# Performance work log

Hardware: AMD Instinct MI355X
Metric: run time of the kernel (lower is better)

## Reference

```python
import jax, jax.numpy as jnp
import numpy as np

B = 128
K = 16
# (in_ch, featdim, dim) per stage, matching conv1..conv11
DIMS = [(3, 8, 2048), (8, 32, 1024), (32, 64, 512), (64, 64, 256), (64, 64, 128),
        (64, 128, 64), (128, 256, 32), (256, 512, 16), (512, 512, 8), (512, 512, 4),
        (512, 1024, 2)]


def setup_inputs() -> dict:
    key = jax.random.key(0)
    ks = jax.random.split(key, 64)
    inp = {"x": jax.random.normal(ks[0], (B, 3, 2048), dtype=jnp.float32)}
    i = 1
    for li, (cin, cf, d) in enumerate(DIMS, start=1):
        inp[f"W{li}"] = jax.random.normal(ks[i], (3 * cf, cin), dtype=jnp.float32) / np.sqrt(cin).astype(np.float32); i += 1
        inp[f"b{li}"] = jax.random.normal(ks[i], (3 * cf,), dtype=jnp.float32) * 0.01; i += 1
        inp[f"sel{li}"] = jax.random.randint(ks[i], (d,), 0, 3); i += 1
    inp["fcW"] = jax.random.normal(ks[i], (K, 1024), dtype=jnp.float32) / np.sqrt(1024).astype(np.float32); i += 1
    inp["fcb"] = jax.random.normal(ks[i], (K,), dtype=jnp.float32) * 0.01
    return inp


def kdconv(x, W, b, sel, featdim, dim):
    # 1x1 conv == per-position matmul: x [B, Cin, dim] -> y [B, 3*featdim, dim]
    y = jax.nn.relu(jnp.einsum('oi,bin->bon', W, x) + b[None, :, None])
    y = y.reshape(-1, featdim, 3, dim)
    # kd split-dim gather: pick one of the 3 feature groups per position
    y = jnp.take_along_axis(y, sel[None, None, None, :], axis=2)[:, :, 0, :]  # [B, featdim, dim]
    # pairwise max-pool of sibling leaves
    return y.reshape(-1, featdim, dim // 2, 2).max(axis=-1)  # [B, featdim, dim//2]


def reference(x, sel1, sel2, sel3, sel4, sel5, sel6, sel7, sel8, sel9, sel10, sel11,
              W1, b1, W2, b2, W3, b3, W4, b4, W5, b5, W6, b6, W7, b7, W8, b8,
              W9, b9, W10, b10, W11, b11, fcW, fcb):
    Ws = [W1, W2, W3, W4, W5, W6, W7, W8, W9, W10, W11]
    bs = [b1, b2, b3, b4, b5, b6, b7, b8, b9, b10, b11]
    sels = [sel1, sel2, sel3, sel4, sel5, sel6, sel7, sel8, sel9, sel10, sel11]
    h = x
    for (cin, cf, d), W, b, s in zip(DIMS, Ws, bs, sels):
        h = kdconv(h, W, b, s, cf, d)
    h = h.reshape(-1, 1024)  # [B, 1024]
    return jax.nn.log_softmax(h @ fcW.T + fcb, axis=-1)
```

## Files before the change

kernel.cpp:

```cpp
#include <hip/hip_runtime.h>
#include <math.h>

typedef __attribute__((ext_vector_type(8))) short bf16x8;
typedef __attribute__((ext_vector_type(4))) float f32x4;

__device__ __forceinline__ unsigned short f2bf(float f) {
    unsigned u = __builtin_bit_cast(unsigned, f);
    u += 0x7FFF + ((u >> 16) & 1);
    return (unsigned short)(u >> 16);
}
__device__ __forceinline__ float bf2f(unsigned short h) {
    unsigned u = ((unsigned)h) << 16;
    return __builtin_bit_cast(float, u);
}

struct K1Params {
    const float* x;
    const float* W1; const float* B1; const int* S1;
    const float* W2; const float* B2; const int* S2;
    const float* Wsrc[9];
    unsigned short* Wb;
    unsigned short* X3;
};

__global__ __launch_bounds__(256) void k1_kernel(K1Params P)
{
    const int tid = threadIdx.x;

    if (blockIdx.x >= 128) {
        int gt = (blockIdx.x - 128) * 256 + tid;
        const int we[9] = {6144, 12288, 12288, 24576, 98304, 393216, 786432, 786432, 1572864};
        int off = 0;
#pragma unroll
        for (int li = 0; li < 9; ++li) {
            const float4* src = (const float4*)P.Wsrc[li];
            ushort4* dst = (ushort4*)(P.Wb + off);
            int n4 = we[li] >> 2;
            for (int i = gt; i < n4; i += 32768) {
                float4 w = src[i];
                dst[i] = make_ushort4(f2bf(w.x), f2bf(w.y), f2bf(w.z), f2bf(w.w));
            }
            off += we[li];
        }
        return;
    }

    __shared__ float wl1[72], bl1[24], wl2[768], bl2[96];
    __shared__ unsigned short bufL1[16 * 64 * 8];

    if (tid < 72) wl1[tid] = P.W1[tid];
    if (tid >= 128 && tid < 152) bl1[tid - 128] = P.B1[tid - 128];
    for (int i = tid; i < 768; i += 256) wl2[i] = P.W2[i];
    if (tid < 96) bl2[tid] = P.B2[tid];
    __syncthreads();

    const int npT = blockIdx.x >> 1;
    const int b0  = (blockIdx.x & 1) * 64;

    for (int i = tid; i < 1024; i += 256) {
        int pos_l = i >> 6, bl = i & 63;
        int np1 = npT * 16 + pos_l;
        int b = b0 + bl;
        int s0 = P.S1[2 * np1], s1 = P.S1[2 * np1 + 1];
        const float* xb = P.x + (size_t)b * 6144 + 2 * np1;
        float2 c0 = *(const float2*)(xb);
        float2 c1 = *(const float2*)(xb + 2048);
        float2 c2 = *(const float2*)(xb + 4096);
        unsigned short o[8];
#pragma unroll
        for (int f = 0; f < 8; ++f) {
            int r0 = f * 3 + s0, r1 = f * 3 + s1;
            float z0 = fmaf(wl1[r0*3+2], c2.x, fmaf(wl1[r0*3+1], c1.x, fmaf(wl1[r0*3+0], c0.x, bl1[r0])));
            float z1 = fmaf(wl1[r1*3+2], c2.y, fmaf(wl1[r1*3+1], c1.y, fmaf(wl1[r1*3+0], c0.y, bl1[r1])));
            o[f] = f2bf(fmaxf(fmaxf(z0, z1), 0.f));
        }
        unsigned short* dst = &bufL1[((size_t)pos_l * 64 + bl) * 8];
        *(ushort4*)dst       = make_ushort4(o[0], o[1], o[2], o[3]);
        *(ushort4*)(dst + 4) = make_ushort4(o[4], o[5], o[6], o[7]);
    }
    __syncthreads();

    for (int i = tid; i < 512; i += 256) {
        int np_l = i >> 6, bl = i & 63;
        int np2 = npT * 8 + np_l;
        int s0 = P.S2[2 * np2], s1 = P.S2[2 * np2 + 1];
        const unsigned short* r0 = &bufL1[((size_t)(2 * np_l) * 64 + bl) * 8];
        const unsigned short* r1 = &bufL1[((size_t)(2 * np_l + 1) * 64 + bl) * 8];
        float xa[8], xb[8];
        {
            ushort4 u0 = *(const ushort4*)r0, u1 = *(const ushort4*)(r0 + 4);
            ushort4 v0 = *(const ushort4*)r1, v1 = *(const ushort4*)(r1 + 4);
            xa[0]=bf2f(u0.x); xa[1]=bf2f(u0.y); xa[2]=bf2f(u0.z); xa[3]=bf2f(u0.w);
            xa[4]=bf2f(u1.x); xa[5]=bf2f(u1.y); xa[6]=bf2f(u1.z); xa[7]=bf2f(u1.w);
            xb[0]=bf2f(v0.x); xb[1]=bf2f(v0.y); xb[2]=bf2f(v0.z); xb[3]=bf2f(v0.w);
            xb[4]=bf2f(v1.x); xb[5]=bf2f(v1.y); xb[6]=bf2f(v1.z); xb[7]=bf2f(v1.w);
        }
        unsigned short o[32];
#pragma unroll
        for (int f = 0; f < 32; ++f) {
            const float* w0 = &wl2[(f * 3 + s0) * 8];
            const float* w1 = &wl2[(f * 3 + s1) * 8];
            float z0 = bl2[f * 3 + s0], z1 = bl2[f * 3 + s1];
#pragma unroll
            for (int k = 0; k < 8; ++k) {
                z0 = fmaf(w0[k], xa[k], z0);
                z1 = fmaf(w1[k], xb[k], z1);
            }
            o[f] = f2bf(fmaxf(fmaxf(z0, z1), 0.f));
        }
        unsigned short* dst = P.X3 + ((size_t)np2 * 128 + b0 + bl) * 32;
#pragma unroll
        for (int i2 = 0; i2 < 8; ++i2)
            *(ushort4*)(dst + 4 * i2) = make_ushort4(o[4*i2], o[4*i2+1], o[4*i2+2], o[4*i2+3]);
    }
}

template<int CIN>
__device__ __forceinline__ void mfma_tile(
    const unsigned short* a0, const unsigned short* a1,
    const unsigned short* b0p, const unsigned short* b1p,
    f32x4& acc0, f32x4& acc1)
{
#pragma unroll
    for (int k = 0; k < CIN; k += 32) {
        bf16x8 A0 = __builtin_bit_cast(bf16x8, *(const float4*)(const void*)(a0 + k));
        bf16x8 A1 = __builtin_bit_cast(bf16x8, *(const float4*)(const void*)(a1 + k));
        bf16x8 B0 = __builtin_bit_cast(bf16x8, *(const float4*)(const void*)(b0p + k));
        bf16x8 B1 = __builtin_bit_cast(bf16x8, *(const float4*)(const void*)(b1p + k));
        acc0 = __builtin_amdgcn_mfma_f32_16x16x32_bf16(A0, B0, acc0, 0, 0, 0);
        acc1 = __builtin_amdgcn_mfma_f32_16x16x32_bf16(A1, B1, acc1, 0, 0, 0);
    }
}

template<int CIN, int RPE>
__device__ __forceinline__ void mfma_tile_lds(
    const unsigned short* a0, const unsigned short* a1,
    const unsigned short* b0p, const unsigned short* b1p,
    f32x4& acc0, f32x4& acc1)
{
#pragma unroll
    for (int k = 0; k < CIN; k += 32) {
        bf16x8 A0 = __builtin_bit_cast(bf16x8, *(const float4*)(const void*)(a0 + k));
        bf16x8 A1 = __builtin_bit_cast(bf16x8, *(const float4*)(const void*)(a1 + k));
        bf16x8 B0 = __builtin_bit_cast(bf16x8, *(const float4*)(const void*)(b0p + k));
        bf16x8 B1 = __builtin_bit_cast(bf16x8, *(const float4*)(const void*)(b1p + k));
        acc0 = __builtin_amdgcn_mfma_f32_16x16x32_bf16(A0, B0, acc0, 0, 0, 0);
        acc1 = __builtin_amdgcn_mfma_f32_16x16x32_bf16(A1, B1, acc1, 0, 0, 0);
    }
}

__device__ __forceinline__ void epilogue_store(
    unsigned short* dst, const f32x4& acc0, const f32x4& acc1,
    const float* bias, int fbase, int s0, int s1)
{
    unsigned short o[4];
#pragma unroll
    for (int r = 0; r < 4; ++r) {
        float v = fmaxf(fmaxf(acc0[r] + bias[(fbase + r) * 3 + s0],
                              acc1[r] + bias[(fbase + r) * 3 + s1]), 0.f);
        o[r] = f2bf(v);
    }
    *(ushort4*)dst = make_ushort4(o[0], o[1], o[2], o[3]);
}

__global__ __launch_bounds__(256) void stage2_kernel(
    const unsigned short* __restrict__ X3,
    const unsigned short* __restrict__ Wb,
    const float* __restrict__ B3, const int* __restrict__ S3,
    const float* __restrict__ B4, const int* __restrict__ S4,
    const float* __restrict__ B5, const int* __restrict__ S5,
    unsigned short* __restrict__ X6)
{
    constexpr int RPE = 72;
    __shared__ unsigned short L3o[4 * 32 * RPE];
    __shared__ unsigned short L4o[2 * 32 * RPE];

    const int tid  = threadIdx.x;
    const int lane = tid & 63;
    const int wv   = tid >> 6;
    const int c = lane & 15, q = lane >> 4;
    const int n5 = blockIdx.x >> 2;
    const int b0 = (blockIdx.x & 3) * 32;

    const unsigned short* W3b = Wb;
    const unsigned short* W4b = Wb + 6144;
    const unsigned short* W5b = Wb + 18432;

    for (int t = wv; t < 32; t += 4) {
        int bt = t & 1, ft = (t >> 1) & 3, j = t >> 3;
        int np = 4 * n5 + j;
        int s0 = __builtin_amdgcn_readfirstlane(S3[2 * np]);
        int s1 = __builtin_amdgcn_readfirstlane(S3[2 * np + 1]);
        int f0 = ft * 16, bl = bt * 16;
        const unsigned short* a0 = W3b + (size_t)((f0 + c) * 3 + s0) * 32 + q * 8;
        const unsigned short* a1 = W3b + (size_t)((f0 + c) * 3 + s1) * 32 + q * 8;
        const unsigned short* bp0 = X3 + ((size_t)(8 * n5 + 2 * j) * 128 + b0 + bl + c) * 32 + q * 8;
        const unsigned short* bp1 = X3 + ((size_t)(8 * n5 + 2 * j + 1) * 128 + b0 + bl + c) * 32 + q * 8;
        f32x4 acc0 = {0.f,0.f,0.f,0.f}, acc1 = {0.f,0.f,0.f,0.f};
        mfma_tile<32>(a0, a1, bp0, bp1, acc0, acc1);
        epilogue_store(&L3o[((size_t)j * 32 + bl + c) * RPE + f0 + q * 4],
                       acc0, acc1, B3, f0 + q * 4, s0, s1);
    }
    __syncthreads();

    for (int t = wv; t < 16; t += 4) {
        int bt = t & 1, ft = (t >> 1) & 3, j = t >> 3;
        int np = 2 * n5 + j;
        int s0 = __builtin_amdgcn_readfirstlane(S4[2 * np]);
        int s1 = __builtin_amdgcn_readfirstlane(S4[2 * np + 1]);
        int f0 = ft * 16, bl = bt * 16;
        const unsigned short* a0 = W4b + (size_t)((f0 + c) * 3 + s0) * 64 + q * 8;
        const unsigned short* a1 = W4b + (size_t)((f0 + c) * 3 + s1) * 64 + q * 8;
        const unsigned short* bp0 = &L3o[((size_t)(2 * j) * 32 + bl + c) * RPE + q * 8];
        const unsigned short* bp1 = &L3o[((size_t)(2 * j + 1) * 32 + bl + c) * RPE + q * 8];
        f32x4 acc0 = {0.f,0.f,0.f,0.f}, acc1 = {0.f,0.f,0.f,0.f};
        mfma_tile_lds<64, RPE>(a0, a1, bp0, bp1, acc0, acc1);
        epilogue_store(&L4o[((size_t)j * 32 + bl + c) * RPE + f0 + q * 4],
                       acc0, acc1, B4, f0 + q * 4, s0, s1);
    }
    __syncthreads();

    for (int t = wv; t < 8; t += 4) {
        int bt = t & 1, ft = t >> 1;
        int s0 = __builtin_amdgcn_readfirstlane(S5[2 * n5]);
        int s1 = __builtin_amdgcn_readfirstlane(S5[2 * n5 + 1]);
        int f0 = ft * 16, bl = bt * 16;
        const unsigned short* a0 = W5b + (size_t)((f0 + c) * 3 + s0) * 64 + q * 8;
        const unsigned short* a1 = W5b + (size_t)((f0 + c) * 3 + s1) * 64 + q * 8;
        const unsigned short* bp0 = &L4o[((size_t)(0) * 32 + bl + c) * RPE + q * 8];
        const unsigned short* bp1 = &L4o[((size_t)(1) * 32 + bl + c) * RPE + q * 8];
        f32x4 acc0 = {0.f,0.f,0.f,0.f}, acc1 = {0.f,0.f,0.f,0.f};
        mfma_tile_lds<64, RPE>(a0, a1, bp0, bp1, acc0, acc1);
        epilogue_store(X6 + ((size_t)n5 * 128 + b0 + bl + c) * 64 + f0 + q * 4,
                       acc0, acc1, B5, f0 + q * 4, s0, s1);
    }
}

template<int CIN, int CF, int NP, int MW, int NW>
__global__ __launch_bounds__(256) void mfma_kernel(
    const unsigned short* __restrict__ Xin,
    const unsigned short* __restrict__ Wb,
    const float* __restrict__ bias,
    const int*   __restrict__ sel,
    unsigned short* __restrict__ Xout)
{
    constexpr int FT = CF / (16 * MW);
    constexpr int BT = 128 / (16 * NW);

    const int wid  = threadIdx.x >> 6;
    const int lane = threadIdx.x & 63;
    const int task = blockIdx.x * 4 + wid;
    const int bi = task % BT;
    const int fi = (task / BT) % FT;
    const int n  = task / (BT * FT);

    const int c = lane & 15;
    const int q = lane >> 4;
    const int s0 = __builtin_amdgcn_readfirstlane(sel[2 * n]);
    const int s1 = __builtin_amdgcn_readfirstlane(sel[2 * n + 1]);

    const int f0 = fi * 16 * MW;
    const int b0 = bi * 16 * NW;

    const unsigned short* ap[2][MW];
    const unsigned short* bp[2][NW];
#pragma unroll
    for (int p = 0; p < 2; ++p) {
        int s = p ? s1 : s0;
#pragma unroll
        for (int mi = 0; mi < MW; ++mi)
            ap[p][mi] = Wb + (size_t)((f0 + mi * 16 + c) * 3 + s) * CIN + q * 8;
#pragma unroll
        for (int ni = 0; ni < NW; ++ni)
            bp[p][ni] = Xin + ((size_t)(2 * n + p) * 128 + b0 + ni * 16 + c) * CIN + q * 8;
    }

    f32x4 acc[2][MW][NW];
#pragma unroll
    for (int p = 0; p < 2; ++p)
#pragma unroll
        for (int mi = 0; mi < MW; ++mi)
#pragma unroll
            for (int ni = 0; ni < NW; ++ni)
                acc[p][mi][ni] = (f32x4){0.f, 0.f, 0.f, 0.f};

#pragma unroll 2
    for (int k = 0; k < CIN; k += 32) {
        bf16x8 A[2][MW], B[2][NW];
#pragma unroll
        for (int p = 0; p < 2; ++p) {
#pragma unroll
            for (int mi = 0; mi < MW; ++mi)
                A[p][mi] = __builtin_bit_cast(bf16x8, *(const float4*)(const void*)(ap[p][mi] + k));
#pragma unroll
            for (int ni = 0; ni < NW; ++ni)
                B[p][ni] = __builtin_bit_cast(bf16x8, *(const float4*)(const void*)(bp[p][ni] + k));
        }
#pragma unroll
        for (int p = 0; p < 2; ++p)
#pragma unroll
            for (int mi = 0; mi < MW; ++mi)
#pragma unroll
                for (int ni = 0; ni < NW; ++ni)
                    acc[p][mi][ni] = __builtin_amdgcn_mfma_f32_16x16x32_bf16(
                        A[p][mi], B[p][ni], acc[p][mi][ni], 0, 0, 0);
    }

#pragma unroll
    for (int mi = 0; mi < MW; ++mi) {
        int fbase = f0 + mi * 16 + q * 4;
#pragma unroll
        for (int ni = 0; ni < NW; ++ni) {
            int b = b0 + ni * 16 + c;
            epilogue_store(Xout + ((size_t)n * 128 + b) * CF + fbase,
                           acc[0][mi][ni], acc[1][mi][ni], bias, fbase, s0, s1);
        }
    }
}

__global__ __launch_bounds__(256) void fc_logsoftmax_kernel(
    const unsigned short* __restrict__ h, const float* __restrict__ fcW,
    const float* __restrict__ fcb, float* __restrict__ out)
{
    int b   = blockIdx.x;
    int tid = threadIdx.x;
    int k     = tid & 15;
    int chunk = tid >> 4;

    const float* __restrict__ wk = fcW + (size_t)k * 1024;
    const unsigned short* hb = h + (size_t)b * 1024;

    float partial = 0.0f;
    int j0 = chunk * 64;
#pragma unroll 8
    for (int j = 0; j < 64; ++j)
        partial = fmaf(bf2f(hb[j0 + j]), wk[j0 + j], partial);

    __shared__ float red[16][17];
    red[chunk][k] = partial;
    __syncthreads();

    __shared__ float logits[16];
    if (tid < 16) {
        float s = fcb[tid];
#pragma unroll
        for (int c = 0; c < 16; ++c) s += red[c][tid];
        logits[tid] = s;
    }
    __syncthreads();

    if (tid < 16) {
        float mx = -INFINITY;
#pragma unroll
        for (int kk = 0; kk < 16; ++kk) mx = fmaxf(mx, logits[kk]);
        float se = 0.0f;
#pragma unroll
        for (int kk = 0; kk < 16; ++kk) se += expf(logits[kk] - mx);
        out[b * 16 + tid] = logits[tid] - mx - logf(se);
    }
}

extern "C" void kernel_launch(void* const* d_in, const int* in_sizes, int n_in,
                              void* d_out, int out_size, void* d_ws, size_t ws_size,
                              hipStream_t stream)
{
#define WL(i) (const float*)d_in[1 + 3 * (i)]
#define BL(i) (const float*)d_in[2 + 3 * (i)]
#define SL(i) (const int*)  d_in[3 + 3 * (i)]

    unsigned short* bufA = (unsigned short*)d_ws;
    unsigned short* bufB = bufA + 2u * 1024u * 1024u;
    unsigned short* Wb   = bufB + 2u * 1024u * 1024u;

    const int o3 = 0, o4 = 6144, o5 = 18432, o6 = 30720, o7 = 55296,
              o8 = 153600, o9 = 546816, o10 = 1333248, o11 = 2119680;
    (void)o3; (void)o4; (void)o5;

    K1Params P;
    P.x = (const float*)d_in[0];
    P.W1 = WL(0); P.B1 = BL(0); P.S1 = SL(0);
    P.W2 = WL(1); P.B2 = BL(1); P.S2 = SL(1);
    for (int i = 0; i < 9; ++i) P.Wsrc[i] = WL(2 + i);
    P.Wb = Wb; P.X3 = bufA;
    k1_kernel<<<256, 256, 0, stream>>>(P);

    stage2_kernel<<<256, 256, 0, stream>>>(bufA, Wb,
        BL(2), SL(2), BL(3), SL(3), BL(4), SL(4), bufB);

    mfma_kernel<64, 128, 32, 2, 2><<<128, 256, 0, stream>>>(bufB, Wb + o6,  BL(5),  SL(5),  bufA);
    mfma_kernel<128, 256, 16, 2, 2><<<128, 256, 0, stream>>>(bufA, Wb + o7,  BL(6),  SL(6),  bufB);
    mfma_kernel<256, 512, 8, 2, 2><<<128, 256, 0, stream>>>(bufB, Wb + o8,  BL(7),  SL(7),  bufA);
    mfma_kernel<512, 512, 4, 1, 2><<<128, 256, 0, stream>>>(bufA, Wb + o9,  BL(8),  SL(8),  bufB);
    mfma_kernel<512, 512, 2, 1, 2><<<64, 256, 0, stream>>>(bufB, Wb + o10, BL(9),  SL(9),  bufA);
    mfma_kernel<512, 1024, 1, 1, 2><<<64, 256, 0, stream>>>(bufA, Wb + o11, BL(10), SL(10), bufB);

    fc_logsoftmax_kernel<<<128, 256, 0, stream>>>(bufB, (const float*)d_in[34], (const float*)d_in[35], (float*)d_out);

#undef WL
#undef BL
#undef SL
}
```

Before: 217.8 us.

## Fuse conv6 and conv7 into one LDS-staged kernel and retile late stages

```diff
diff --git a/kernel.cpp b/kernel.cpp
--- a/kernel.cpp
+++ b/kernel.cpp
@@ -132,23 +132,6 @@
     }
 }
 
-template<int CIN, int RPE>
-__device__ __forceinline__ void mfma_tile_lds(
-    const unsigned short* a0, const unsigned short* a1,
-    const unsigned short* b0p, const unsigned short* b1p,
-    f32x4& acc0, f32x4& acc1)
-{
-#pragma unroll
-    for (int k = 0; k < CIN; k += 32) {
-        bf16x8 A0 = __builtin_bit_cast(bf16x8, *(const float4*)(const void*)(a0 + k));
-        bf16x8 A1 = __builtin_bit_cast(bf16x8, *(const float4*)(const void*)(a1 + k));
-        bf16x8 B0 = __builtin_bit_cast(bf16x8, *(const float4*)(const void*)(b0p + k));
-        bf16x8 B1 = __builtin_bit_cast(bf16x8, *(const float4*)(const void*)(b1p + k));
-        acc0 = __builtin_amdgcn_mfma_f32_16x16x32_bf16(A0, B0, acc0, 0, 0, 0);
-        acc1 = __builtin_amdgcn_mfma_f32_16x16x32_bf16(A1, B1, acc1, 0, 0, 0);
-    }
-}
-
 __device__ __forceinline__ void epilogue_store(
     unsigned short* dst, const f32x4& acc0, const f32x4& acc1,
     const float* bias, int fbase, int s0, int s1)
@@ -214,7 +197,7 @@
         const unsigned short* bp0 = &L3o[((size_t)(2 * j) * 32 + bl + c) * RPE + q * 8];
         const unsigned short* bp1 = &L3o[((size_t)(2 * j + 1) * 32 + bl + c) * RPE + q * 8];
         f32x4 acc0 = {0.f,0.f,0.f,0.f}, acc1 = {0.f,0.f,0.f,0.f};
-        mfma_tile_lds<64, RPE>(a0, a1, bp0, bp1, acc0, acc1);
+        mfma_tile<64>(a0, a1, bp0, bp1, acc0, acc1);
         epilogue_store(&L4o[((size_t)j * 32 + bl + c) * RPE + f0 + q * 4],
                        acc0, acc1, B4, f0 + q * 4, s0, s1);
     }
@@ -230,9 +213,59 @@
         const unsigned short* bp0 = &L4o[((size_t)(0) * 32 + bl + c) * RPE + q * 8];
         const unsigned short* bp1 = &L4o[((size_t)(1) * 32 + bl + c) * RPE + q * 8];
         f32x4 acc0 = {0.f,0.f,0.f,0.f}, acc1 = {0.f,0.f,0.f,0.f};
-        mfma_tile_lds<64, RPE>(a0, a1, bp0, bp1, acc0, acc1);
+        mfma_tile<64>(a0, a1, bp0, bp1, acc0, acc1);
         epilogue_store(X6 + ((size_t)n5 * 128 + b0 + bl + c) * 64 + f0 + q * 4,
                        acc0, acc1, B5, f0 + q * 4, s0, s1);
+    }
+}
+
+__global__ __launch_bounds__(512) void stage67_kernel(
+    const unsigned short* __restrict__ X6,
+    const unsigned short* __restrict__ W6b, const float* __restrict__ B6, const int* __restrict__ S6,
+    const unsigned short* __restrict__ W7b, const float* __restrict__ B7, const int* __restrict__ S7,
+    unsigned short* __restrict__ X8)
+{
+    constexpr int RPE = 136;
+    __shared__ unsigned short L6o[2 * 16 * RPE];
+
+    const int tid  = threadIdx.x;
+    const int lane = tid & 63;
+    const int wv   = tid >> 6;
+    const int c = lane & 15, q = lane >> 4;
+    const int n7 = blockIdx.x >> 3;
+    const int b0 = (blockIdx.x & 7) * 16;
+
+    for (int t = wv; t < 16; t += 8) {
+        int j = t >> 3, ft = t & 7;
+        int np = 2 * n7 + j;
+        int s0 = __builtin_amdgcn_readfirstlane(S6[2 * np]);
+        int s1 = __builtin_amdgcn_readfirstlane(S6[2 * np + 1]);
+        int f0 = ft * 16;
+        const unsigned short* a0 = W6b + (size_t)((f0 + c) * 3 + s0) * 64 + q * 8;
+        const unsigned short* a1 = W6b + (size_t)((f0 + c) * 3 + s1) * 64 + q * 8;
+        const unsigned short* bp0 = X6 + ((size_t)(2 * np) * 128 + b0 + c) * 64 + q * 8;
+        const unsigned short* bp1 = X6 + ((size_t)(2 * np + 1) * 128 + b0 + c) * 64 + q * 8;
+        f32x4 acc0 = {0.f,0.f,0.f,0.f}, acc1 = {0.f,0.f,0.f,0.f};
+        mfma_tile<64>(a0, a1, bp0, bp1, acc0, acc1);
+        epilogue_store(&L6o[((size_t)j * 16 + c) * RPE + f0 + q * 4],
+                       acc0, acc1, B6, f0 + q * 4, s0, s1);
+    }
+    __syncthreads();
+
+    {
+        int s0 = __builtin_amdgcn_readfirstlane(S7[2 * n7]);
+        int s1 = __builtin_amdgcn_readfirstlane(S7[2 * n7 + 1]);
+        for (int t = wv; t < 16; t += 8) {
+            int f0 = t * 16;
+            const unsigned short* a0 = W7b + (size_t)((f0 + c) * 3 + s0) * 128 + q * 8;
+            const unsigned short* a1 = W7b + (size_t)((f0 + c) * 3 + s1) * 128 + q * 8;
+            const unsigned short* bp0 = &L6o[((size_t)(0) * 16 + c) * RPE + q * 8];
+            const unsigned short* bp1 = &L6o[((size_t)(1) * 16 + c) * RPE + q * 8];
+            f32x4 acc0 = {0.f,0.f,0.f,0.f}, acc1 = {0.f,0.f,0.f,0.f};
+            mfma_tile<128>(a0, a1, bp0, bp1, acc0, acc1);
+            epilogue_store(X8 + ((size_t)n7 * 128 + b0 + c) * 256 + f0 + q * 4,
+                           acc0, acc1, B7, f0 + q * 4, s0, s1);
+        }
     }
 }
 
@@ -372,9 +405,8 @@
     unsigned short* bufB = bufA + 2u * 1024u * 1024u;
     unsigned short* Wb   = bufB + 2u * 1024u * 1024u;
 
-    const int o3 = 0, o4 = 6144, o5 = 18432, o6 = 30720, o7 = 55296,
-              o8 = 153600, o9 = 546816, o10 = 1333248, o11 = 2119680;
-    (void)o3; (void)o4; (void)o5;
+    const int o6 = 30720, o7 = 55296, o8 = 153600,
+              o9 = 546816, o10 = 1333248, o11 = 2119680;
 
     K1Params P;
     P.x = (const float*)d_in[0];
@@ -387,14 +419,15 @@
     stage2_kernel<<<256, 256, 0, stream>>>(bufA, Wb,
         BL(2), SL(2), BL(3), SL(3), BL(4), SL(4), bufB);
 
-    mfma_kernel<64, 128, 32, 2, 2><<<128, 256, 0, stream>>>(bufB, Wb + o6,  BL(5),  SL(5),  bufA);
-    mfma_kernel<128, 256, 16, 2, 2><<<128, 256, 0, stream>>>(bufA, Wb + o7,  BL(6),  SL(6),  bufB);
-    mfma_kernel<256, 512, 8, 2, 2><<<128, 256, 0, stream>>>(bufB, Wb + o8,  BL(7),  SL(7),  bufA);
-    mfma_kernel<512, 512, 4, 1, 2><<<128, 256, 0, stream>>>(bufA, Wb + o9,  BL(8),  SL(8),  bufB);
-    mfma_kernel<512, 512, 2, 1, 2><<<64, 256, 0, stream>>>(bufB, Wb + o10, BL(9),  SL(9),  bufA);
-    mfma_kernel<512, 1024, 1, 1, 2><<<64, 256, 0, stream>>>(bufA, Wb + o11, BL(10), SL(10), bufB);
-
-    fc_logsoftmax_kernel<<<128, 256, 0, stream>>>(bufB, (const float*)d_in[34], (const float*)d_in[35], (float*)d_out);
+    stage67_kernel<<<128, 512, 0, stream>>>(bufB,
+        Wb + o6, BL(5), SL(5), Wb + o7, BL(6), SL(6), bufA);
+
+    mfma_kernel<256, 512, 8, 2, 2><<<128, 256, 0, stream>>>(bufA, Wb + o8,  BL(7),  SL(7),  bufB);
+    mfma_kernel<512, 512, 4, 1, 1><<<256, 256, 0, stream>>>(bufB, Wb + o9,  BL(8),  SL(8),  bufA);
+    mfma_kernel<512, 512, 2, 1, 1><<<128, 256, 0, stream>>>(bufA, Wb + o10, BL(9),  SL(9),  bufB);
+    mfma_kernel<512, 1024, 1, 1, 1><<<128, 256, 0, stream>>>(bufB, Wb + o11, BL(10), SL(10), bufA);
+
+    fc_logsoftmax_kernel<<<128, 256, 0, stream>>>(bufA, (const float*)d_in[34], (const float*)d_in[35], (float*)d_out);
 
 #undef WL
 #undef BL
```

After: 212.7 us. 2.3% less time.
